# Kernel tuning notes

Measured on AMD Instinct MI355X. Metric: run time of the kernel, lower is better.

## Reference

```python
import jax, jax.numpy as jnp
import numpy as np


def binarize(x):
    # sign to +/-1 (>=0 -> 1); forward value only (STE handled in bwd module)
    return jnp.where(x >= 0, 1.0, -1.0).astype(x.dtype)


def setup_inputs() -> dict:
    key = jax.random.key(0)
    k1, k2, k3 = jax.random.split(key, 3)
    B, D_IN, D_H, D_OUT = 16384, 4096, 4096, 1
    x = jax.random.normal(k1, (B, D_IN), dtype=jnp.float32)
    W1 = jax.random.normal(k2, (D_H, D_IN), dtype=jnp.float32) * 0.02
    W2 = jax.random.normal(k3, (D_OUT, D_H), dtype=jnp.float32) * 0.02
    return {"x": x, "W1": W1, "W2": W2}


def reference(x, W1, W2):
    # fc1: BinaryLinear (binarized weight, no bias) + BinaryTanh (hardtanh then sign)
    h = x @ binarize(W1).T                      # [B, D_H]
    h = binarize(jnp.clip(h, -1.0, 1.0))        # hardtanh + binarize -> +/-1
    # fc2: BinaryLinear + Sigmoid
    out = jax.nn.sigmoid(h @ binarize(W2).T)    # [B, 1]
    y_hat = jnp.squeeze((out >= 0.5).astype(jnp.float32))  # [B]
    return out, y_hat
```

## Files before the change

### kernel.cpp

```cpp
#include <hip/hip_runtime.h>
#include <stdint.h>


typedef int v4i  __attribute__((ext_vector_type(4)));
typedef int v16i __attribute__((ext_vector_type(16)));

#define B_ROWS   16384
#define DIM      4096
#define MT       64
#define NT       128
#define KT       64

__global__ void pack_x_kernel(float* __restrict__ x) {
    const int b = blockIdx.x, t = threadIdx.x;
    float* row = x + (size_t)b * DIM;
    float f[16];
#pragma unroll
    for (int i = 0; i < 4; ++i) {
        float4 v = ((const float4*)(row + t * 16))[i];
        f[i*4+0] = v.x; f[i*4+1] = v.y; f[i*4+2] = v.z; f[i*4+3] = v.w;
    }
    __syncthreads();
    uint32_t wds[4][4];
#pragma unroll
    for (int j = 0; j < 4; ++j) {
#pragma unroll
        for (int d = 0; d < 4; ++d) wds[d][j] = 0u;
#pragma unroll
        for (int i = 0; i < 4; ++i) {
            int v = __double2int_rn((double)f[j*4+i] * 67108864.0);
#pragma unroll
            for (int d = 0; d < 4; ++d) {
                int bb = (int)(int8_t)(v & 0xff);
                wds[d][j] |= (uint32_t)(bb & 0xff) << (8 * i);
                v = (v - bb) >> 8;
            }
        }
    }
    int8_t* rowb = (int8_t*)row;
#pragma unroll
    for (int d = 0; d < 4; ++d) {
        int4 o; o.x = (int)wds[d][0]; o.y = (int)wds[d][1];
        o.z = (int)wds[d][2]; o.w = (int)wds[d][3];
        *(int4*)(rowb + d * DIM + t * 16) = o;
    }
}

__global__ void pack_w1_kernel(const float* __restrict__ W1, int8_t* __restrict__ wsB) {
    const int tg = blockIdx.x * 256 + threadIdx.x;
    const int n  = tg >> 8;
    const int k0 = (tg & 255) << 4;
    const float* src = W1 + (size_t)n * DIM + k0;
    uint32_t w[4];
#pragma unroll
    for (int j = 0; j < 4; ++j) {
        float4 v = ((const float4*)src)[j];
        uint32_t b0 = (v.x >= 0.f) ? 0x01u : 0xFFu;
        uint32_t b1 = (v.y >= 0.f) ? 0x01u : 0xFFu;
        uint32_t b2 = (v.z >= 0.f) ? 0x01u : 0xFFu;
        uint32_t b3 = (v.w >= 0.f) ? 0x01u : 0xFFu;
        w[j] = b0 | (b1 << 8) | (b2 << 16) | (b3 << 24);
    }
    const int nb = n >> 7, kt = k0 >> 6;
    const int nsub = (n >> 5) & 3, ks = (k0 >> 5) & 1;
    const int L = (n & 31) | (((k0 >> 4) & 1) << 5);
    const size_t off = ((size_t)(nb * 64 + kt) << 13) + (nsub << 11) + (ks << 10) + (L << 4);
    int4 o; o.x = (int)w[0]; o.y = (int)w[1]; o.z = (int)w[2]; o.w = (int)w[3];
    *(int4*)(wsB + off) = o;
}

__global__ void pack_w2_kernel(const float* __restrict__ W2, int8_t* __restrict__ w2s) {
    const int j = blockIdx.x * 256 + threadIdx.x;
    if (j < DIM) w2s[j] = (W2[j] >= 0.f) ? (int8_t)1 : (int8_t)-1;
}

__launch_bounds__(256, 2)
__global__ void gemm_kernel(const int8_t* __restrict__ xq,
                            const int8_t* __restrict__ wsB,
                            const int8_t* __restrict__ w2s,
                            int* __restrict__ logit) {
    __shared__ __align__(16) int8_t aT[4 * MT * KT];
    __shared__ __align__(16) int8_t bT[NT * KT];

    const int bid = blockIdx.x;
    const int nb = bid & 31, mb = bid >> 5;
    const int t = threadIdx.x, lane = t & 63, w = t >> 6;
    const int wy = w >> 1, wx = w & 1;

    v16i acc[2][4];
#pragma unroll
    for (int n = 0; n < 2; ++n)
#pragma unroll
        for (int d = 0; d < 4; ++d)
#pragma unroll
            for (int i = 0; i < 16; ++i) acc[n][d][i] = 0;

    const int8_t* aSrc = xq + (size_t)(mb * MT + lane) * (4 * DIM) + w * DIM;
    const int8_t* bSrc = wsB + ((size_t)(nb * 64) << 13) + t * 32;
    const int aDst = w * (MT * KT) + ((lane >> 5) << 11) + ((lane & 31) << 4);

    for (int kt = 0; kt < DIM / KT; ++kt) {
#pragma unroll
        for (int k16 = 0; k16 < 4; ++k16) {
            v4i v = *(const v4i*)(aSrc + kt * KT + k16 * 16);
            *(v4i*)(aT + aDst + ((k16 >> 1) << 10) + ((k16 & 1) << 9)) = v;
        }
        {
            const v4i* s = (const v4i*)(bSrc + ((size_t)kt << 13));
            *(v4i*)(bT + t * 32)      = s[0];
            *(v4i*)(bT + t * 32 + 16) = s[1];
        }
        __syncthreads();
#pragma unroll
        for (int s = 0; s < 2; ++s) {
            v4i af[4], bf[2];
#pragma unroll
            for (int d = 0; d < 4; ++d)
                af[d] = *(const v4i*)(aT + d * (MT * KT) + (wy << 11) + (s << 10) + (lane << 4));
#pragma unroll
            for (int n = 0; n < 2; ++n)
                bf[n] = *(const v4i*)(bT + ((wx * 2 + n) << 11) + (s << 10) + (lane << 4));
#pragma unroll
            for (int n = 0; n < 2; ++n)
#pragma unroll
                for (int d = 0; d < 4; ++d)
                    acc[n][d] = __builtin_amdgcn_mfma_i32_32x32x32_i8(af[d], bf[n], acc[n][d], 0, 0, 0);
        }
        __syncthreads();
    }

    const int half = lane >> 5, col = lane & 31;
    int psum[16];
#pragma unroll
    for (int r = 0; r < 16; ++r) psum[r] = 0;
#pragma unroll
    for (int n = 0; n < 2; ++n) {
        const int j = nb * NT + wx * 64 + n * 32 + col;
        const int w2v = (int)w2s[j];
#pragma unroll
        for (int r = 0; r < 16; ++r) {
            long long h = (long long)acc[n][0][r]
                        + ((long long)acc[n][1][r] << 8)
                        + ((long long)acc[n][2][r] << 16)
                        + ((long long)acc[n][3][r] << 24);
            psum[r] += (h >= 0) ? w2v : -w2v;
        }
    }
#pragma unroll
    for (int r = 0; r < 16; ++r) {
#pragma unroll
        for (int m = 1; m <= 16; m <<= 1)
            psum[r] += __shfl_xor(psum[r], m, 64);
    }
    if (col == 0) {
        const int rowBase = mb * MT + wy * 32 + 4 * half;
#pragma unroll
        for (int r = 0; r < 16; ++r)
            atomicAdd(logit + rowBase + (r & 3) + 8 * (r >> 2), psum[r]);
    }
}

__global__ void finalize_kernel(const int* __restrict__ logit, float* __restrict__ out) {
    const int b = blockIdx.x * 256 + threadIdx.x;
    if (b < B_ROWS) {
        const int l = logit[b];
        out[b]          = 1.f / (1.f + expf(-(float)l));
        out[B_ROWS + b] = (l >= 0) ? 1.f : 0.f;
    }
}

extern "C" void kernel_launch(void* const* d_in, const int* in_sizes, int n_in,
                              void* d_out, int out_size, void* d_ws, size_t ws_size,
                              hipStream_t stream) {
    float*       x   = (float*)d_in[0];
    const float* W1  = (const float*)d_in[1];
    const float* W2  = (const float*)d_in[2];
    float*       out = (float*)d_out;

    int8_t* ws   = (int8_t*)d_ws;
    int*    logit = (int*)ws;
    int8_t* w2s  = ws + 65536;
    int8_t* wsB  = ws + 69632;

    hipMemsetAsync(logit, 0, B_ROWS * sizeof(int), stream);
    pack_x_kernel<<<B_ROWS, 256, 0, stream>>>(x);
    pack_w1_kernel<<<DIM, 256, 0, stream>>>(W1, wsB);
    pack_w2_kernel<<<16, 256, 0, stream>>>(W2, w2s);
    gemm_kernel<<<(B_ROWS / MT) * (DIM / NT), 256, 0, stream>>>(
        (const int8_t*)x, wsB, w2s, logit);
    finalize_kernel<<<B_ROWS / 256, 256, 0, stream>>>(logit, out);
}
```

Baseline: 1.789 ms.

## Pre-pack x into MFMA fragment layout and stream B via async LDS DMA

Measured after the change: 2.005 ms. +12.1%, slower.

```diff
diff --git a/kernel.cpp b/kernel.cpp
--- a/kernel.cpp
+++ b/kernel.cpp
@@ -11,6 +11,45 @@
 #define NT       128
 #define KT       64
 
+#define WS_LOGIT  0
+#define WS_W2S    65536
+#define WS_B      69632
+#define WS_A      (69632 + 16777216)
+#define WS_NEEDED ((size_t)WS_A + 268435456ULL)
+
+__device__ __forceinline__ void dma16(const void* g, void* l) {
+    __builtin_amdgcn_global_load_lds(
+        (const __attribute__((address_space(1))) void*)g,
+        (__attribute__((address_space(3))) void*)l, 16, 0, 0);
+}
+
+__global__ void pack_x_frag_kernel(const float* __restrict__ x, int8_t* __restrict__ wsA) {
+    const int mb32 = blockIdx.x, t = threadIdx.x;
+    const int d = t >> 6, kh = (t >> 5) & 1, mm = t & 31;
+    const float* srcBase = x + ((size_t)(mb32 * 32 + mm) << 12) + (kh << 4);
+    int8_t* dst = wsA + ((size_t)mb32 << 19) + (t << 4);
+    for (int ks32 = 0; ks32 < 128; ++ks32) {
+        const float4* s4 = (const float4*)(srcBase + (ks32 << 5));
+        uint32_t wds[4];
+#pragma unroll
+        for (int j = 0; j < 4; ++j) {
+            float4 f = s4[j];
+            float fv[4] = {f.x, f.y, f.z, f.w};
+            uint32_t a = 0;
+#pragma unroll
+            for (int i = 0; i < 4; ++i) {
+                int v = __float2int_rn(fv[i] * 67108864.0f);
+                int b = (int)(int8_t)(v & 0xff);
+                for (int step = 0; step < d; ++step) { v = (v - b) >> 8; b = (int)(int8_t)(v & 0xff); }
+                a |= ((uint32_t)(b & 0xff)) << (8 * i);
+            }
+            wds[j] = a;
+        }
+        int4 o; o.x = (int)wds[0]; o.y = (int)wds[1]; o.z = (int)wds[2]; o.w = (int)wds[3];
+        *(int4*)(dst + ((size_t)ks32 << 12)) = o;
+    }
+}
+
 __global__ void pack_x_kernel(float* __restrict__ x) {
     const int b = blockIdx.x, t = threadIdx.x;
     float* row = x + (size_t)b * DIM;
@@ -28,7 +67,7 @@
         for (int d = 0; d < 4; ++d) wds[d][j] = 0u;
 #pragma unroll
         for (int i = 0; i < 4; ++i) {
-            int v = __double2int_rn((double)f[j*4+i] * 67108864.0);
+            int v = __float2int_rn(f[j*4+i] * 67108864.0f);
 #pragma unroll
             for (int d = 0; d < 4; ++d) {
                 int bb = (int)(int8_t)(v & 0xff);
@@ -75,6 +114,95 @@
 }
 
 __launch_bounds__(256, 2)
+__global__ void gemm_direct_kernel(const int8_t* __restrict__ wsA,
+                                   const int8_t* __restrict__ wsB,
+                                   const int8_t* __restrict__ w2s,
+                                   int* __restrict__ logit) {
+    __shared__ __align__(16) int8_t bT[2][8192];
+
+    const int bid = blockIdx.x;
+    const int nb = bid & 31, mb = bid >> 5;
+    const int t = threadIdx.x, lane = t & 63, w = t >> 6;
+    const int wy = w >> 1, wx = w & 1;
+
+    v16i acc[2][4];
+#pragma unroll
+    for (int n = 0; n < 2; ++n)
+#pragma unroll
+        for (int d = 0; d < 4; ++d)
+#pragma unroll
+            for (int i = 0; i < 16; ++i) acc[n][d][i] = 0;
+
+    const int8_t* aBase = wsA + ((size_t)(mb * 2 + wy) << 19) + (lane << 4);
+    const int8_t* bSrcL = wsB + ((size_t)(nb * 64) << 13) + (w << 11) + (lane << 4);
+
+    dma16(bSrcL,        &bT[0][w << 11]);
+    dma16(bSrcL + 1024, &bT[0][(w << 11) + 1024]);
+
+#pragma unroll 2
+    for (int kt = 0; kt < 64; ++kt) {
+        __syncthreads();
+        if (kt < 63) {
+            const int8_t* s = bSrcL + ((size_t)(kt + 1) << 13);
+            int8_t* dst = &bT[(kt + 1) & 1][w << 11];
+            dma16(s,        dst);
+            dma16(s + 1024, dst + 1024);
+        }
+        const int8_t* aKt = aBase + ((size_t)kt << 13);
+        v4i af[2][4];
+#pragma unroll
+        for (int s = 0; s < 2; ++s)
+#pragma unroll
+            for (int d = 0; d < 4; ++d)
+                af[s][d] = *(const v4i*)(aKt + (s << 12) + (d << 10));
+        const int8_t* bCur = &bT[kt & 1][(wx << 12) + (lane << 4)];
+        v4i bf[2][2];
+#pragma unroll
+        for (int s = 0; s < 2; ++s)
+#pragma unroll
+            for (int n = 0; n < 2; ++n)
+                bf[s][n] = *(const v4i*)(bCur + (n << 11) + (s << 10));
+#pragma unroll
+        for (int s = 0; s < 2; ++s)
+#pragma unroll
+            for (int n = 0; n < 2; ++n)
+#pragma unroll
+                for (int d = 0; d < 4; ++d)
+                    acc[n][d] = __builtin_amdgcn_mfma_i32_32x32x32_i8(af[s][d], bf[s][n], acc[n][d], 0, 0, 0);
+    }
+
+    const int half = lane >> 5, col = lane & 31;
+    int psum[16];
+#pragma unroll
+    for (int r = 0; r < 16; ++r) psum[r] = 0;
+#pragma unroll
+    for (int n = 0; n < 2; ++n) {
+        const int j = nb * NT + wx * 64 + n * 32 + col;
+        const int w2v = (int)w2s[j];
+#pragma unroll
+        for (int r = 0; r < 16; ++r) {
+            long long h = (long long)acc[n][0][r]
+                        + ((long long)acc[n][1][r] << 8)
+                        + ((long long)acc[n][2][r] << 16)
+                        + ((long long)acc[n][3][r] << 24);
+            psum[r] += (h >= 0) ? w2v : -w2v;
+        }
+    }
+#pragma unroll
+    for (int r = 0; r < 16; ++r) {
+#pragma unroll
+        for (int m = 1; m <= 16; m <<= 1)
+            psum[r] += __shfl_xor(psum[r], m, 64);
+    }
+    if (col == 0) {
+        const int rowBase = mb * MT + wy * 32 + 4 * half;
+#pragma unroll
+        for (int r = 0; r < 16; ++r)
+            atomicAdd(logit + rowBase + (r & 3) + 8 * (r >> 2), psum[r]);
+    }
+}
+
+__launch_bounds__(256, 2)
 __global__ void gemm_kernel(const int8_t* __restrict__ xq,
                             const int8_t* __restrict__ wsB,
                             const int8_t* __restrict__ w2s,
@@ -177,16 +305,22 @@
     const float* W2  = (const float*)d_in[2];
     float*       out = (float*)d_out;
 
-    int8_t* ws   = (int8_t*)d_ws;
-    int*    logit = (int*)ws;
-    int8_t* w2s  = ws + 65536;
-    int8_t* wsB  = ws + 69632;
+    int8_t* ws    = (int8_t*)d_ws;
+    int*    logit = (int*)(ws + WS_LOGIT);
+    int8_t* w2s   = ws + WS_W2S;
+    int8_t* wsB   = ws + WS_B;
 
     hipMemsetAsync(logit, 0, B_ROWS * sizeof(int), stream);
-    pack_x_kernel<<<B_ROWS, 256, 0, stream>>>(x);
     pack_w1_kernel<<<DIM, 256, 0, stream>>>(W1, wsB);
     pack_w2_kernel<<<16, 256, 0, stream>>>(W2, w2s);
-    gemm_kernel<<<(B_ROWS / MT) * (DIM / NT), 256, 0, stream>>>(
-        (const int8_t*)x, wsB, w2s, logit);
+
+    if (ws_size >= WS_NEEDED) {
+        int8_t* wsA = ws + WS_A;
+        pack_x_frag_kernel<<<B_ROWS / 32, 256, 0, stream>>>(x, wsA);
+        gemm_direct_kernel<<<(B_ROWS / MT) * (DIM / NT), 256, 0, stream>>>(wsA, wsB, w2s, logit);
+    } else {
+        pack_x_kernel<<<B_ROWS, 256, 0, stream>>>(x);
+        gemm_kernel<<<(B_ROWS / MT) * (DIM / NT), 256, 0, stream>>>((const int8_t*)x, wsB, w2s, logit);
+    }
     finalize_kernel<<<B_ROWS / 256, 256, 0, stream>>>(logit, out);
 }
```
